# Kernel tuning notes

Hardware: AMD Instinct MI355X
Metric: run time of the kernel (lower is better)

Reference implementation:

```python
import jax, jax.numpy as jnp
import numpy as np
from jax import lax

S, B, H, V = 1024, 32, 512, 32000  # seq_len, batch, hidden, vocab


def setup_inputs() -> dict:
    key = jax.random.key(0)
    ks = jax.random.split(key, 12)
    d = {"word_inputs": jax.random.randint(ks[0], (S, B), 0, V)}
    d["embedding"] = jax.random.normal(ks[1], (V, H), jnp.float32) * 0.02
    s = 1.0 / np.sqrt(H)
    i = 2
    for n in ["fwd1", "fwd2", "bwd1", "bwd2"]:
        d[f"W_ih_{n}"] = jax.random.uniform(ks[i], (4 * H, H), jnp.float32, -s, s); i += 1
        d[f"W_hh_{n}"] = jax.random.uniform(ks[i], (4 * H, H), jnp.float32, -s, s); i += 1
        d[f"b_ih_{n}"] = jnp.zeros((4 * H,), jnp.float32)
        d[f"b_hh_{n}"] = jnp.zeros((4 * H,), jnp.float32)
    return d


def _lstm_step(x, h, c, W_ih, W_hh, b, mask):
    # torch.nn.LSTMCell gate order: i, f, g, o
    g = x @ W_ih.T + h @ W_hh.T + b  # [B, 4H]
    i_, f_, g_, o_ = jnp.split(g, 4, axis=-1)
    c_new = jax.nn.sigmoid(f_) * c + jax.nn.sigmoid(i_) * jnp.tanh(g_)
    h_new = jax.nn.sigmoid(o_) * jnp.tanh(c_new)
    m = mask[:, None]  # mask True => keep old state (padding step)
    return jnp.where(m, h, h_new), jnp.where(m, c, c_new)


def _run_direction(emb, masks, p1, p2):
    z = jnp.zeros((emb.shape[1], p1[0].shape[0] // 4), emb.dtype)

    def step(carry, xm):
        h1, c1, h2, c2 = carry
        x, m = xm
        h1, c1 = _lstm_step(x, h1, c1, p1[0], p1[1], p1[2], m)
        h2, c2 = _lstm_step(h1, h2, c2, p2[0], p2[1], p2[2], m)
        return (h1, c1, h2, c2), h2

    carry, hs = lax.scan(step, (z, z, z, z), (emb, masks))
    return hs, carry


def reference(word_inputs, embedding,
              W_ih_fwd1, W_hh_fwd1, b_ih_fwd1, b_hh_fwd1,
              W_ih_fwd2, W_hh_fwd2, b_ih_fwd2, b_hh_fwd2,
              W_ih_bwd1, W_hh_bwd1, b_ih_bwd1, b_hh_bwd1,
              W_ih_bwd2, W_hh_bwd2, b_ih_bwd2, b_hh_bwd2):
    # dropout in eval mode (identity) for a deterministic reference
    emb = embedding[word_inputs]           # [S, B, H]
    masks = word_inputs == 1               # padding token id == 1
    p_f1 = (W_ih_fwd1, W_hh_fwd1, b_ih_fwd1 + b_hh_fwd1)
    p_f2 = (W_ih_fwd2, W_hh_fwd2, b_ih_fwd2 + b_hh_fwd2)
    p_b1 = (W_ih_bwd1, W_hh_bwd1, b_ih_bwd1 + b_hh_bwd1)
    p_b2 = (W_ih_bwd2, W_hh_bwd2, b_ih_bwd2 + b_hh_bwd2)
    fhs, _ = _run_direction(emb, masks, p_f1, p_f2)
    bhs, bcarry = _run_direction(emb[::-1], masks[::-1], p_b1, p_b2)
    # original: outputs[i] = fhs[i] + reversed(bhs)[i] / 2  (note: only bwd halved)
    outputs = fhs + bhs[::-1] / 2
    bh1, bc1, bh2, bc2 = bcarry  # final backward states (bstatus1, bstatus2)
    return outputs, bh1, bc1, bh2, bc2
```

## Files before the change

### kernel.cpp

```cpp
#include <hip/hip_runtime.h>
#include <math.h>


#define SEQ 1024
#define NB 32
#define NH 512
#define BH (NB*NH)
#define NV 32000
#define KP 1032

typedef __attribute__((ext_vector_type(8))) short short8;
typedef __attribute__((ext_vector_type(4))) float f32x4;
typedef unsigned long long u64;

struct P {
  const int*   word;
  const float* emb;
  const float* Wih[4];
  const float* Whh[4];
  const float* bih[4];
  const float* bhh[4];
  unsigned* flags;
  unsigned* gen;
  unsigned* hpk;
  const unsigned* embP;
  float* out;
};

__device__ __forceinline__ unsigned short f2bf(float x) {
  unsigned u = __float_as_uint(x);
  return (unsigned short)((u + 0x7fffu + ((u >> 16) & 1u)) >> 16);
}
__device__ __forceinline__ float bf2f(unsigned short b) {
  return __uint_as_float(((unsigned)b) << 16);
}
__device__ __forceinline__ float sigf(float x) { return 1.0f / (1.0f + expf(-x)); }

__device__ __forceinline__ unsigned ald(const unsigned* p_) {
  return __hip_atomic_load((unsigned*)p_, __ATOMIC_RELAXED, __HIP_MEMORY_SCOPE_AGENT);
}
__device__ __forceinline__ u64 ald64(const u64* p_) {
  return __hip_atomic_load((u64*)p_, __ATOMIC_RELAXED, __HIP_MEMORY_SCOPE_AGENT);
}
__device__ __forceinline__ void ast(unsigned* p_, unsigned v) {
  __hip_atomic_store(p_, v, __ATOMIC_RELAXED, __HIP_MEMORY_SCOPE_AGENT);
}
__device__ __forceinline__ float aldf(const float* p_) {
  return __hip_atomic_load((float*)p_, __ATOMIC_RELAXED, __HIP_MEMORY_SCOPE_AGENT);
}
__device__ __forceinline__ void astf(float* p_, float v) {
  __hip_atomic_store(p_, v, __ATOMIC_RELAXED, __HIP_MEMORY_SCOPE_AGENT);
}

__device__ __forceinline__ void stage_slab(const unsigned* slab,
                                           unsigned short* xhHi,
                                           unsigned short* xhLo,
                                           int Lpair, int koff) {
  const u64* s64 = (const u64*)slab;
  u64 A[32];
#pragma unroll
  for (int q = 0; q < 32; ++q) A[q] = ald64(s64 + Lpair + q * 128);
#pragma unroll
  for (int q = 0; q < 32; ++q) {
    const int r = q >> 1;
    const int c = (q & 1) * 128 + Lpair;
    const unsigned w0 = (unsigned)A[q];
    const unsigned w1 = (unsigned)(A[q] >> 32);
    *(unsigned*)(xhHi + r * KP + koff + 2 * c) = (w0 & 0xffffu) | (w1 << 16);
    *(unsigned*)(xhLo + r * KP + koff + 2 * c) = (w0 >> 16)     | (w1 & 0xffff0000u);
  }
}

__global__ void conv_embp(const float* __restrict__ e,
                          unsigned* __restrict__ pk) {
  const size_t i = ((size_t)blockIdx.x * 256 + threadIdx.x) * 8;
  float4 a = *(const float4*)(e + i);
  float4 b = *(const float4*)(e + i + 4);
  float xs[8] = {a.x, a.y, a.z, a.w, b.x, b.y, b.z, b.w};
  unsigned o[8];
#pragma unroll
  for (int q = 0; q < 8; ++q) {
    unsigned short hb = f2bf(xs[q]);
    unsigned short lb = f2bf(xs[q] - bf2f(hb));
    o[q] = (unsigned)hb | ((unsigned)lb << 16);
  }
  uint4 v0, v1;
  v0.x=o[0]; v0.y=o[1]; v0.z=o[2]; v0.w=o[3];
  v1.x=o[4]; v1.y=o[5]; v1.z=o[6]; v1.w=o[7];
  *(uint4*)(pk + i)     = v0;
  *(uint4*)(pk + i + 4) = v1;
}

__global__ __launch_bounds__(256, 1) void enc_persist(P p) {
  extern __shared__ unsigned short smem[];
  unsigned short* xhHi = smem;
  unsigned short* xhLo = smem + 16 * KP;
  float* gl2 = (float*)(smem + 32 * KP);

  const int tid  = threadIdx.x;
  const int bid  = blockIdx.x;
  const int dl   = bid >> 6;
  const int dir  = dl >> 1, layer = dl & 1;
  const int r6   = bid & 63;
  const int u0   = (r6 >> 1) * 16;
  const int b0   = (r6 & 1) * 16;
  const int lane = tid & 63, wv = tid >> 6;

  short8 aHi[32], aLo[32];
  {
    const int kg = (lane >> 4) * 8;
#pragma unroll
    for (int gg = 0; gg < 4; ++gg) {
      const int gr = gg * 512 + u0 + (lane & 15);
      const float* Wi = p.Wih[dl] + (size_t)gr * NH;
      const float* Wh = p.Whh[dl] + (size_t)gr * NH;
#pragma unroll
      for (int kk = 0; kk < 8; ++kk) {
        const int k0 = (wv * 8 + kk) * 32 + kg;
        const float* s = (k0 < 512) ? (Wi + k0) : (Wh + (k0 - 512));
        float4 v0 = *(const float4*)s;
        float4 v1 = *(const float4*)(s + 4);
        float xs[8] = {v0.x, v0.y, v0.z, v0.w, v1.x, v1.y, v1.z, v1.w};
        short8 h8, l8;
#pragma unroll
        for (int q = 0; q < 8; ++q) {
          unsigned short hb = f2bf(xs[q]);
          h8[q] = (short)hb;
          l8[q] = (short)f2bf(xs[q] - bf2f(hb));
        }
        aHi[gg * 8 + kk] = h8; aLo[gg * 8 + kk] = l8;
      }
    }
  }

  const int cu = tid & 15, cb = tid >> 4;
  const int uG = u0 + cu;
  const float bi  = p.bih[dl][uG]        + p.bhh[dl][uG];
  const float bf_ = p.bih[dl][512 + uG]  + p.bhh[dl][512 + uG];
  const float bg  = p.bih[dl][1024 + uG] + p.bhh[dl][1024 + uG];
  const float bo  = p.bih[dl][1536 + uG] + p.bhh[dl][1536 + uG];

  float c_reg = 0.f, h_reg = 0.f;

  const int sr = tid >> 4;
  const int rb = tid & 15;
  const int ks = sr * 64;

  const int rp = tid >> 3;
  const int lp = tid & 7;

  int tk, tk_st, tk_pk;
  {
    const int to0 = dir ? (SEQ - 1) : 0;
    tk    = p.word[(size_t)to0 * NB + b0 + cb];
    tk_st = p.word[(size_t)to0 * NB + b0 + rb];
    tk_pk = p.word[(size_t)to0 * NB + b0 + (rp & 15)];
  }

  const bool use_pk = (layer == 0) && (tid < 128) && (p.embP != nullptr);
  const bool do_epf = (layer == 0) && (sr < 8) && (p.embP == nullptr);
  union { float4 f[16]; uint4 u[16]; } epr;
  if (use_pk) {
    const uint4* src = (const uint4*)(p.embP + (size_t)tk_pk * NH);
#pragma unroll
    for (int q = 0; q < 16; ++q) epr.u[q] = src[lp + q * 8];
  } else if (do_epf) {
    const float* e = p.emb + (size_t)tk_st * NH + ks;
#pragma unroll
    for (int q = 0; q < 16; ++q) epr.f[q] = *(const float4*)(e + q * 4);
  }

  for (int j = 0; j <= SEQ; ++j) {
    const int act = layer ? (j >= 1) : (j < SEQ);
    const int t = layer ? (j - 1) : j;
    const int torig = dir ? (SEQ - 1 - t) : t;
    const int par = j & 1;

    if (act) {
      if (wv < 2) {
        if (layer == 0) {
          if (p.embP) {
#pragma unroll
            for (int q = 0; q < 16; ++q) {
              const uint4 w = epr.u[q];
              const int u = 4 * (lp + q * 8);
              uint2 hv, lv;
              hv.x = (w.x & 0xffffu) | (w.y << 16);
              hv.y = (w.z & 0xffffu) | (w.w << 16);
              lv.x = (w.x >> 16)     | (w.y & 0xffff0000u);
              lv.y = (w.z >> 16)     | (w.w & 0xffff0000u);
              *(uint2*)(xhHi + rp * KP + u) = hv;
              *(uint2*)(xhLo + rp * KP + u) = lv;
            }
          } else {
#pragma unroll
            for (int h2 = 0; h2 < 2; ++h2) {
#pragma unroll
              for (int q = 0; q < 4; ++q) {
                const float4 va = epr.f[h2 * 8 + 2 * q];
                const float4 vb = epr.f[h2 * 8 + 2 * q + 1];
                float xs[8] = {va.x, va.y, va.z, va.w, vb.x, vb.y, vb.z, vb.w};
                unsigned hw[4], lw[4];
#pragma unroll
                for (int m = 0; m < 4; ++m) {
                  unsigned short ha = f2bf(xs[2*m]);
                  unsigned short hc = f2bf(xs[2*m+1]);
                  unsigned short la = f2bf(xs[2*m]   - bf2f(ha));
                  unsigned short lc = f2bf(xs[2*m+1] - bf2f(hc));
                  hw[m] = (unsigned)ha | ((unsigned)hc << 16);
                  lw[m] = (unsigned)la | ((unsigned)lc << 16);
                }
                uint4 hv, lv;
                hv.x=hw[0]; hv.y=hw[1]; hv.z=hw[2]; hv.w=hw[3];
                lv.x=lw[0]; lv.y=lw[1]; lv.z=lw[2]; lv.w=lw[3];
                *(uint4*)(xhHi + rb * KP + ks + h2 * 32 + q * 8) = hv;
                *(uint4*)(xhLo + rb * KP + ks + h2 * 32 + q * 8) = lv;
              }
            }
          }
        } else {
          const unsigned* slab = p.hpk + (size_t)((dl - 1) * 2 + par) * BH
                                       + (size_t)b0 * NH;
          stage_slab(slab, xhHi, xhLo, tid, 0);
        }
      } else {
        const unsigned* slab = p.hpk + (size_t)(dl * 2 + par) * BH
                                     + (size_t)b0 * NH;
        stage_slab(slab, xhHi, xhLo, tid - 128, 512);
      }
    }

    int tk_nx = tk, tk_st_nx = tk_st, tk_pk_nx = tk_pk;
    if (j < SEQ) {
      int t_nx = layer ? j : (j + 1);
      if (t_nx > SEQ - 1) t_nx = SEQ - 1;
      const int to_nx = dir ? (SEQ - 1 - t_nx) : t_nx;
      tk_nx    = p.word[(size_t)to_nx * NB + b0 + cb];
      tk_st_nx = p.word[(size_t)to_nx * NB + b0 + rb];
      tk_pk_nx = p.word[(size_t)to_nx * NB + b0 + (rp & 15)];
    }

    float out_pf = 0.f;
    size_t oi = 0;
    int do_add = 0;
    if (act && layer == 1) {
      oi = (size_t)torig * BH + (size_t)(b0 + cb) * NH + uG;
      do_add = dir ? (torig < 512) : (torig > 511);
      if (do_add) out_pf = aldf(p.out + oi);
    }

    __syncthreads();

    if (act) {
      f32x4 aA[4], aBC[4];
#pragma unroll
      for (int gg = 0; gg < 4; ++gg) {
        aA[gg]  = (f32x4){0.f, 0.f, 0.f, 0.f};
        aBC[gg] = (f32x4){0.f, 0.f, 0.f, 0.f};
      }
      const unsigned short* bp = xhHi + (lane & 15) * KP + (lane >> 4) * 8;
      const unsigned short* bq = xhLo + (lane & 15) * KP + (lane >> 4) * 8;
#pragma unroll
      for (int kk = 0; kk < 8; ++kk) {
        const int kc = wv * 8 + kk;
        short8 bH = *(const short8*)(bp + kc * 32);
        short8 bL = *(const short8*)(bq + kc * 32);
#pragma unroll
        for (int gg = 0; gg < 4; ++gg) {
          aA[gg]  = __builtin_amdgcn_mfma_f32_16x16x32_bf16(aHi[gg*8+kk], bH, aA[gg],  0, 0, 0);
          aBC[gg] = __builtin_amdgcn_mfma_f32_16x16x32_bf16(aLo[gg*8+kk], bH, aBC[gg], 0, 0, 0);
          aBC[gg] = __builtin_amdgcn_mfma_f32_16x16x32_bf16(aHi[gg*8+kk], bL, aBC[gg], 0, 0, 0);
        }
      }
#pragma unroll
      for (int gg = 0; gg < 4; ++gg) {
        f32x4 acc = aA[gg] + aBC[gg];
        *(f32x4*)&gl2[((wv * 4 + gg) * 16 + (lane & 15)) * 20 + (lane >> 4) * 4] = acc;
      }
    }
    __syncthreads();

    if (act) {
#define GL2(w_,g_) gl2[(((w_) * 4 + (g_)) * 16 + cb) * 20 + cu]
      const float vi = ((GL2(0,0)+GL2(1,0)) + (GL2(2,0)+GL2(3,0))) + bi;
      const float vf = ((GL2(0,1)+GL2(1,1)) + (GL2(2,1)+GL2(3,1))) + bf_;
      const float vg = ((GL2(0,2)+GL2(1,2)) + (GL2(2,2)+GL2(3,2))) + bg;
      const float vo = ((GL2(0,3)+GL2(1,3)) + (GL2(2,3)+GL2(3,3))) + bo;
#undef GL2
      float cn = sigf(vf) * c_reg + sigf(vi) * tanhf(vg);
      float hn = sigf(vo) * tanhf(cn);
      if (tk == 1) { cn = c_reg; hn = h_reg; }
      c_reg = cn; h_reg = hn;
      const unsigned short hh = f2bf(hn);
      const unsigned short hl = f2bf(hn - bf2f(hh));
      const size_t hix = (size_t)(dl * 2 + (par ^ 1)) * BH + (size_t)(b0 + cb) * NH + uG;
      ast(p.hpk + hix, (unsigned)hh | ((unsigned)hl << 16));
      if (layer == 1) {
        const float v = dir ? (0.5f * hn) : hn;
        astf(p.out + oi, do_add ? (out_pf + v) : v);
      }
    }

    tk = tk_nx; tk_st = tk_st_nx; tk_pk = tk_pk_nx;

    __syncthreads();
    if (tid == 0)
      ast(p.flags + (size_t)bid * 16, (unsigned)(j + 1));

    if (j + 1 < SEQ) {
      if (use_pk) {
        const uint4* src = (const uint4*)(p.embP + (size_t)tk_pk * NH);
#pragma unroll
        for (int q = 0; q < 16; ++q) epr.u[q] = src[lp + q * 8];
      } else if (do_epf) {
        const float* e = p.emb + (size_t)tk_st * NH + ks;
#pragma unroll
        for (int q = 0; q < 16; ++q) epr.f[q] = *(const float4*)(e + q * 4);
      }
    }

    if (bid == 0) {
      unsigned* f = p.flags + (size_t)tid * 16;
      while (ald(f) < (unsigned)(j + 1)) __builtin_amdgcn_s_sleep(1);
      __syncthreads();
      if (tid == 0) ast(p.gen, (unsigned)(j + 1));
    } else {
      if (tid < 64) {
        while (ald(p.gen) < (unsigned)(j + 1)) __builtin_amdgcn_s_sleep(1);
      }
      __syncthreads();
    }
  }

  if (dl == 2) {
    p.out[(size_t)SEQ * BH + 0 * (size_t)BH + (size_t)(b0 + cb) * NH + uG] = h_reg;
    p.out[(size_t)SEQ * BH + 1 * (size_t)BH + (size_t)(b0 + cb) * NH + uG] = c_reg;
  } else if (dl == 3) {
    p.out[(size_t)SEQ * BH + 2 * (size_t)BH + (size_t)(b0 + cb) * NH + uG] = h_reg;
    p.out[(size_t)SEQ * BH + 3 * (size_t)BH + (size_t)(b0 + cb) * NH + uG] = c_reg;
  }
}

extern "C" void kernel_launch(void* const* d_in, const int* in_sizes, int n_in,
                              void* d_out, int out_size, void* d_ws, size_t ws_size,
                              hipStream_t stream) {
  P p;
  p.word = (const int*)d_in[0];
  p.emb  = (const float*)d_in[1];
  for (int i = 0; i < 4; ++i) {
    p.Wih[i] = (const float*)d_in[2 + i * 4 + 0];
    p.Whh[i] = (const float*)d_in[2 + i * 4 + 1];
    p.bih[i] = (const float*)d_in[2 + i * 4 + 2];
    p.bhh[i] = (const float*)d_in[2 + i * 4 + 3];
  }
  unsigned char* ws = (unsigned char*)d_ws;
  p.flags = (unsigned*)ws;
  p.gen   = (unsigned*)(ws + 16384);
  p.hpk   = (unsigned*)(ws + 16448);
  const size_t embOff  = (size_t)1 << 20;
  const size_t embBytes = (size_t)NV * NH * 4;
  if (ws_size >= embOff + embBytes) {
    p.embP = (const unsigned*)(ws + embOff);
  } else {
    p.embP = nullptr;
  }
  p.out = (float*)d_out;

  hipMemsetAsync(d_ws, 0, 16448 + (size_t)8 * BH * 4, stream);

  if (p.embP) {
    hipLaunchKernelGGL(conv_embp, dim3(8000), dim3(256), 0, stream,
                       p.emb, (unsigned*)p.embP);
  }

  const int smem = 90112;
  hipFuncSetAttribute(reinterpret_cast<const void*>(enc_persist),
                      hipFuncAttributeMaxDynamicSharedMemorySize, smem);
  hipLaunchKernelGGL(enc_persist, dim3(256), dim3(256), smem, stream, p);
}
```

Measured before the change: 4.759 ms.

## Make LDS staging wave-local to drop pre-MFMA barrier and pack flags

The hidden-state slab and embedding staging are remapped so each wave writes exactly the LDS region its own MFMA k-chunk reads. This allows the __syncthreads before the matmul to be skipped when the packed embedding path is used. Per-block arrival flags are also packed contiguously instead of padded to 64-byte strides, so block 0's polling touches fewer cache lines. The risks are correctness if any wave reads LDS data staged by another wave, and more false sharing on the packed flags.

After: 8.496 ms. +78.5%, slower.

```diff
diff --git a/kernel.cpp b/kernel.cpp
--- a/kernel.cpp
+++ b/kernel.cpp
@@ -52,18 +52,21 @@
   __hip_atomic_store(p_, v, __ATOMIC_RELAXED, __HIP_MEMORY_SCOPE_AGENT);
 }
 
-__device__ __forceinline__ void stage_slab(const unsigned* slab,
-                                           unsigned short* xhHi,
-                                           unsigned short* xhLo,
-                                           int Lpair, int koff) {
+__device__ __forceinline__ void stage_slab_wave(const unsigned* slab,
+                                                unsigned short* xhHi,
+                                                unsigned short* xhLo,
+                                                int L, int wvHalf, int koff) {
   const u64* s64 = (const u64*)slab;
   u64 A[32];
 #pragma unroll
-  for (int q = 0; q < 32; ++q) A[q] = ald64(s64 + Lpair + q * 128);
+  for (int q = 0; q < 32; ++q) {
+    const int idx = (q >> 1) * 256 + wvHalf * 128 + (q & 1) * 64 + L;
+    A[q] = ald64(s64 + idx);
+  }
 #pragma unroll
   for (int q = 0; q < 32; ++q) {
     const int r = q >> 1;
-    const int c = (q & 1) * 128 + Lpair;
+    const int c = wvHalf * 128 + (q & 1) * 64 + L;
     const unsigned w0 = (unsigned)A[q];
     const unsigned w1 = (unsigned)(A[q] >> 32);
     *(unsigned*)(xhHi + r * KP + koff + 2 * c) = (w0 & 0xffffu) | (w1 << 16);
@@ -146,24 +149,25 @@
   const int rb = tid & 15;
   const int ks = sr * 64;
 
-  const int rp = tid >> 3;
-  const int lp = tid & 7;
-
-  int tk, tk_st, tk_pk;
+  const int er   = lane >> 2;
+  const int lsub = lane & 3;
+  const int ubase = 256 * wv;
+
+  int tk, tk_st, tk_u;
   {
     const int to0 = dir ? (SEQ - 1) : 0;
     tk    = p.word[(size_t)to0 * NB + b0 + cb];
     tk_st = p.word[(size_t)to0 * NB + b0 + rb];
-    tk_pk = p.word[(size_t)to0 * NB + b0 + (rp & 15)];
-  }
-
-  const bool use_pk = (layer == 0) && (tid < 128) && (p.embP != nullptr);
+    tk_u  = p.word[(size_t)to0 * NB + b0 + er];
+  }
+
+  const bool use_pk = (layer == 0) && (wv < 2) && (p.embP != nullptr);
   const bool do_epf = (layer == 0) && (sr < 8) && (p.embP == nullptr);
   union { float4 f[16]; uint4 u[16]; } epr;
   if (use_pk) {
-    const uint4* src = (const uint4*)(p.embP + (size_t)tk_pk * NH);
-#pragma unroll
-    for (int q = 0; q < 16; ++q) epr.u[q] = src[lp + q * 8];
+    const unsigned* src = p.embP + (size_t)tk_u * NH + ubase + lsub * 4;
+#pragma unroll
+    for (int q = 0; q < 16; ++q) epr.u[q] = *(const uint4*)(src + 16 * q);
   } else if (do_epf) {
     const float* e = p.emb + (size_t)tk_st * NH + ks;
 #pragma unroll
@@ -183,14 +187,14 @@
 #pragma unroll
             for (int q = 0; q < 16; ++q) {
               const uint4 w = epr.u[q];
-              const int u = 4 * (lp + q * 8);
+              const int u = ubase + lsub * 4 + 16 * q;
               uint2 hv, lv;
               hv.x = (w.x & 0xffffu) | (w.y << 16);
               hv.y = (w.z & 0xffffu) | (w.w << 16);
               lv.x = (w.x >> 16)     | (w.y & 0xffff0000u);
               lv.y = (w.z >> 16)     | (w.w & 0xffff0000u);
-              *(uint2*)(xhHi + rp * KP + u) = hv;
-              *(uint2*)(xhLo + rp * KP + u) = lv;
+              *(uint2*)(xhHi + er * KP + u) = hv;
+              *(uint2*)(xhLo + er * KP + u) = lv;
             }
           } else {
 #pragma unroll
@@ -221,23 +225,23 @@
         } else {
           const unsigned* slab = p.hpk + (size_t)((dl - 1) * 2 + par) * BH
                                        + (size_t)b0 * NH;
-          stage_slab(slab, xhHi, xhLo, tid, 0);
+          stage_slab_wave(slab, xhHi, xhLo, lane, wv & 1, 0);
         }
       } else {
         const unsigned* slab = p.hpk + (size_t)(dl * 2 + par) * BH
                                      + (size_t)b0 * NH;
-        stage_slab(slab, xhHi, xhLo, tid - 128, 512);
-      }
-    }
-
-    int tk_nx = tk, tk_st_nx = tk_st, tk_pk_nx = tk_pk;
+        stage_slab_wave(slab, xhHi, xhLo, lane, wv & 1, 512);
+      }
+    }
+
+    int tk_nx = tk, tk_st_nx = tk_st, tk_u_nx = tk_u;
     if (j < SEQ) {
       int t_nx = layer ? j : (j + 1);
       if (t_nx > SEQ - 1) t_nx = SEQ - 1;
       const int to_nx = dir ? (SEQ - 1 - t_nx) : t_nx;
       tk_nx    = p.word[(size_t)to_nx * NB + b0 + cb];
       tk_st_nx = p.word[(size_t)to_nx * NB + b0 + rb];
-      tk_pk_nx = p.word[(size_t)to_nx * NB + b0 + (rp & 15)];
+      tk_u_nx  = p.word[(size_t)to_nx * NB + b0 + er];
     }
 
     float out_pf = 0.f;
@@ -249,7 +253,7 @@
       if (do_add) out_pf = aldf(p.out + oi);
     }
 
-    __syncthreads();
+    if (!p.embP) __syncthreads();
 
     if (act) {
       f32x4 aA[4], aBC[4];
@@ -301,17 +305,17 @@
       }
     }
 
-    tk = tk_nx; tk_st = tk_st_nx; tk_pk = tk_pk_nx;
+    tk = tk_nx; tk_st = tk_st_nx; tk_u = tk_u_nx;
 
     __syncthreads();
     if (tid == 0)
-      ast(p.flags + (size_t)bid * 16, (unsigned)(j + 1));
+      ast(p.flags + bid, (unsigned)(j + 1));
 
     if (j + 1 < SEQ) {
       if (use_pk) {
-        const uint4* src = (const uint4*)(p.embP + (size_t)tk_pk * NH);
-#pragma unroll
-        for (int q = 0; q < 16; ++q) epr.u[q] = src[lp + q * 8];
+        const unsigned* src = p.embP + (size_t)tk_u * NH + ubase + lsub * 4;
+#pragma unroll
+        for (int q = 0; q < 16; ++q) epr.u[q] = *(const uint4*)(src + 16 * q);
       } else if (do_epf) {
         const float* e = p.emb + (size_t)tk_st * NH + ks;
 #pragma unroll
@@ -320,8 +324,7 @@
     }
 
     if (bid == 0) {
-      unsigned* f = p.flags + (size_t)tid * 16;
-      while (ald(f) < (unsigned)(j + 1)) __builtin_amdgcn_s_sleep(1);
+      while (ald(p.flags + tid) < (unsigned)(j + 1)) __builtin_amdgcn_s_sleep(1);
       __syncthreads();
       if (tid == 0) ast(p.gen, (unsigned)(j + 1));
     } else {
```

## Split global grid barrier into per-direction/batch-half sync domains with separate merge

Applied to the files above, without the earlier changes.

Replaces the single 256-block grid-wide barrier with four independent barrier domains (direction × batch half), each of 64 blocks with its own leader and generation counter. Because forward and backward directions no longer share a barrier, the in-kernel read-add on the output is dropped. The backward outputs go to a workspace buffer and a separate merge kernel adds them into the output. This shortens each per-step barrier and decouples directions, at the cost of an extra 128MB buffer write/read pass and a kernel launch.

New measurement: 4.729 ms. No clear change (-0.6%).

```diff
diff --git a/kernel.cpp b/kernel.cpp
--- a/kernel.cpp
+++ b/kernel.cpp
@@ -25,6 +25,7 @@
   unsigned* hpk;
   const unsigned* embP;
   float* out;
+  float* bwd;
 };
 
 __device__ __forceinline__ unsigned short f2bf(float x) {
@@ -89,6 +90,14 @@
   v1.x=o[4]; v1.y=o[5]; v1.z=o[6]; v1.w=o[7];
   *(uint4*)(pk + i)     = v0;
   *(uint4*)(pk + i + 4) = v1;
+}
+
+__global__ void merge_out(float* __restrict__ out, const float* __restrict__ bwd) {
+  const size_t i = ((size_t)blockIdx.x * 256 + threadIdx.x) * 4;
+  float4 a = *(const float4*)(out + i);
+  const float4 b = *(const float4*)(bwd + i);
+  a.x += b.x; a.y += b.y; a.z += b.z; a.w += b.w;
+  *(float4*)(out + i) = a;
 }
 
 __global__ __launch_bounds__(256, 1) void enc_persist(P p) {
@@ -105,6 +114,12 @@
   const int u0   = (r6 >> 1) * 16;
   const int b0   = (r6 & 1) * 16;
   const int lane = tid & 63, wv = tid >> 6;
+
+  const int dom  = p.bwd ? (dir * 2 + (r6 & 1)) : 0;
+  const int lid  = p.bwd ? (layer * 32 + (r6 >> 1)) : bid;
+  unsigned* genp = p.gen + dom * 16;
+  const bool leader = (lid == 0);
+  const int dsz  = p.bwd ? 64 : 256;
 
   short8 aHi[32], aLo[32];
   {
@@ -245,8 +260,10 @@
     int do_add = 0;
     if (act && layer == 1) {
       oi = (size_t)torig * BH + (size_t)(b0 + cb) * NH + uG;
-      do_add = dir ? (torig < 512) : (torig > 511);
-      if (do_add) out_pf = aldf(p.out + oi);
+      if (!p.bwd) {
+        do_add = dir ? (torig < 512) : (torig > 511);
+        if (do_add) out_pf = aldf(p.out + oi);
+      }
     }
 
     __syncthreads();
@@ -296,8 +313,13 @@
       const size_t hix = (size_t)(dl * 2 + (par ^ 1)) * BH + (size_t)(b0 + cb) * NH + uG;
       ast(p.hpk + hix, (unsigned)hh | ((unsigned)hl << 16));
       if (layer == 1) {
-        const float v = dir ? (0.5f * hn) : hn;
-        astf(p.out + oi, do_add ? (out_pf + v) : v);
+        if (p.bwd) {
+          if (dir) astf(p.bwd + oi, 0.5f * hn);
+          else     astf(p.out + oi, hn);
+        } else {
+          const float v = dir ? (0.5f * hn) : hn;
+          astf(p.out + oi, do_add ? (out_pf + v) : v);
+        }
       }
     }
 
@@ -305,7 +327,7 @@
 
     __syncthreads();
     if (tid == 0)
-      ast(p.flags + (size_t)bid * 16, (unsigned)(j + 1));
+      ast(p.flags + (size_t)(dom * 64 + lid) * 16, (unsigned)(j + 1));
 
     if (j + 1 < SEQ) {
       if (use_pk) {
@@ -319,14 +341,16 @@
       }
     }
 
-    if (bid == 0) {
-      unsigned* f = p.flags + (size_t)tid * 16;
-      while (ald(f) < (unsigned)(j + 1)) __builtin_amdgcn_s_sleep(1);
+    if (leader) {
+      if (tid < dsz) {
+        unsigned* f = p.flags + (size_t)(dom * 64 + tid) * 16;
+        while (ald(f) < (unsigned)(j + 1)) __builtin_amdgcn_s_sleep(1);
+      }
       __syncthreads();
-      if (tid == 0) ast(p.gen, (unsigned)(j + 1));
+      if (tid == 0) ast(genp, (unsigned)(j + 1));
     } else {
       if (tid < 64) {
-        while (ald(p.gen) < (unsigned)(j + 1)) __builtin_amdgcn_s_sleep(1);
+        while (ald(genp) < (unsigned)(j + 1)) __builtin_amdgcn_s_sleep(1);
       }
       __syncthreads();
     }
@@ -356,17 +380,18 @@
   unsigned char* ws = (unsigned char*)d_ws;
   p.flags = (unsigned*)ws;
   p.gen   = (unsigned*)(ws + 16384);
-  p.hpk   = (unsigned*)(ws + 16448);
-  const size_t embOff  = (size_t)1 << 20;
+  p.hpk   = (unsigned*)(ws + 16896);
+  const size_t embOff   = (size_t)1 << 20;
   const size_t embBytes = (size_t)NV * NH * 4;
-  if (ws_size >= embOff + embBytes) {
-    p.embP = (const unsigned*)(ws + embOff);
-  } else {
-    p.embP = nullptr;
-  }
+  p.embP = (ws_size >= embOff + embBytes) ? (const unsigned*)(ws + embOff)
+                                          : nullptr;
+  const size_t bwdOff   = (size_t)65 << 20;
+  const size_t bwdBytes = (size_t)SEQ * BH * 4;
+  const bool split = (ws_size >= bwdOff + bwdBytes) && (p.embP != nullptr);
+  p.bwd = split ? (float*)(ws + bwdOff) : nullptr;
   p.out = (float*)d_out;
 
-  hipMemsetAsync(d_ws, 0, 16448 + (size_t)8 * BH * 4, stream);
+  hipMemsetAsync(d_ws, 0, 16896 + (size_t)8 * BH * 4, stream);
 
   if (p.embP) {
     hipLaunchKernelGGL(conv_embp, dim3(8000), dim3(256), 0, stream,
@@ -377,4 +402,9 @@
   hipFuncSetAttribute(reinterpret_cast<const void*>(enc_persist),
                       hipFuncAttributeMaxDynamicSharedMemorySize, smem);
   hipLaunchKernelGGL(enc_persist, dim3(256), dim3(256), smem, stream, p);
-}
+
+  if (split) {
+    hipLaunchKernelGGL(merge_out, dim3(16384), dim3(256), 0, stream,
+                       p.out, p.bwd);
+  }
+}
```
